# Performance work log

Measured on AMD Instinct MI355X. Metric: run time of the kernel, lower is better.

## Reference

```python
import jax, jax.numpy as jnp
import numpy as np

HEADS = 8
DIM_HEAD = 32
SCALE = DIM_HEAD ** -0.5
EPS = 1e-12  # F.normalize eps


def _rmsnorm_ch(t, g):
    # F.normalize(t, dim=1) * g * sqrt(C)  (normalize_dim=1)
    c = t.shape[1]
    norm = jnp.sqrt(jnp.sum(t * t, axis=1, keepdims=True))
    return t / jnp.maximum(norm, EPS) * g[None, :, None, None] * (c ** 0.5)


def setup_inputs() -> dict:
    key = jax.random.key(0)
    ks = jax.random.split(key, 4)
    B, C, H, W = 16, 256, 64, 64
    hidden = HEADS * DIM_HEAD  # 256
    x = jax.random.normal(ks[0], (B, C, H, W), dtype=jnp.float32)
    g1 = jnp.ones((C,), dtype=jnp.float32)
    # conv 1x1 weights stored as [out_ch, in_ch]
    w_qkv = jax.random.normal(ks[1], (hidden * 3, C), dtype=jnp.float32) * (1.0 / np.sqrt(C))
    w_out = jax.random.normal(ks[2], (C, hidden), dtype=jnp.float32) * (1.0 / np.sqrt(hidden))
    b_out = jnp.zeros((C,), dtype=jnp.float32)
    g2 = jnp.ones((C,), dtype=jnp.float32)
    return {"x": x, "g1": g1, "w_qkv": w_qkv, "w_out": w_out, "b_out": b_out, "g2": g2}


def reference(x, g1, w_qkv, w_out, b_out, g2):
    b, c, h, w = x.shape
    n = h * w
    xn = _rmsnorm_ch(x, g1)
    # 1x1 conv (no bias) == channel matmul
    qkv = jnp.einsum('oc,bchw->bohw', w_qkv, xn)
    q, k, v = jnp.split(qkv, 3, axis=1)
    # b (h c) x y -> b h c (x y)
    q = q.reshape(b, HEADS, DIM_HEAD, n)
    k = k.reshape(b, HEADS, DIM_HEAD, n)
    v = v.reshape(b, HEADS, DIM_HEAD, n)
    q = jax.nn.softmax(q, axis=-2) * SCALE  # softmax over dim_head
    k = jax.nn.softmax(k, axis=-1)          # softmax over sequence
    context = jnp.einsum('bhdn,bhen->bhde', k, v)  # [b,h,d,e] small
    out = jnp.einsum('bhde,bhdn->bhen', context, q)
    out = out.reshape(b, HEADS * DIM_HEAD, h, w)
    out = jnp.einsum('oc,bchw->bohw', w_out, out) + b_out[None, :, None, None]
    return _rmsnorm_ch(out, g2) + x
```

## Files before the change

### kernel.cpp

```cpp
#include <hip/hip_runtime.h>
#include <math.h>


#define B_ 16
#define C_ 256
#define N_ 4096
#define SCALE_ 0.17677669529663687f
#define EPS_ 1e-12f

typedef __attribute__((ext_vector_type(8))) short bf16x8;
typedef __attribute__((ext_vector_type(4))) float f32x4;

__device__ __forceinline__ ushort f2bf(float f) {
    union { float f; uint u; } x; x.f = f;
    uint r = (x.u + 0x7FFFu + ((x.u >> 16) & 1u)) >> 16;
    return (ushort)r;
}
__device__ __forceinline__ float bf2f(ushort s) {
    union { uint u; float f; } x; x.u = ((uint)s) << 16;
    return x.f;
}

__global__ __launch_bounds__(256) void k_prep(const float* __restrict__ w_qkv,
                                              const float* __restrict__ g1,
                                              ushort* __restrict__ Wp) {
    int o = blockIdx.x, c = threadIdx.x;
    Wp[(size_t)o * 256 + c] = f2bf(w_qkv[(size_t)o * 256 + c] * g1[c]);
}

__global__ __launch_bounds__(512) void k_kvctx(const ushort* __restrict__ Wp,
                                               const float* __restrict__ x,
                                               float* __restrict__ ctxp,
                                               float* __restrict__ sums_p) {
    extern __shared__ char lds[];
    ushort (*Asub)[40] = (ushort(*)[40])lds;
    char* BQ = lds + 20480;
    char* P  = lds + 86016;
    float* sspA  = (float*)(lds + 151552);
    float* rinvA = (float*)(lds + 153600);
    const int b = blockIdx.y, s = blockIdx.x;
    const int col0 = s * 128;
    const int t = threadIdx.x, l = t & 63, w = t >> 6;
    const int lr = l & 15, grp = l >> 4;
    const int wn = w & 3, wo = w >> 2;
    const float* xb = x + (size_t)b * C_ * N_ + col0;

    {
        int col = t & 127, rg = t >> 7;
        float ss = 0.f;
        #pragma unroll 8
        for (int i = 0; i < 64; ++i) {
            float v = xb[(size_t)(rg * 64 + i) * N_ + col];
            ss += v * v;
        }
        sspA[rg * 128 + col] = ss;
    }
    __syncthreads();
    if (t < 128)
        rinvA[t] = 16.f / fmaxf(sqrtf(sspA[t] + sspA[128 + t] + sspA[256 + t] + sspA[384 + t]), EPS_);
    __syncthreads();
    {
        int col = t & 127, rg = t >> 7;
        float rv = rinvA[col];
        uint sw = (uint)((col & 7) << 4);
        #pragma unroll
        for (int i = 0; i < 16; ++i) {
            int c = rg * 64 + i * 4;
            uint2 pk;
            pk.x = (uint)f2bf(xb[(size_t)c * N_ + col] * rv)
                 | ((uint)f2bf(xb[(size_t)(c + 1) * N_ + col] * rv) << 16);
            pk.y = (uint)f2bf(xb[(size_t)(c + 2) * N_ + col] * rv)
                 | ((uint)f2bf(xb[(size_t)(c + 3) * N_ + col] * rv) << 16);
            *(uint2*)(BQ + (((uint)(col * 512 + c * 2)) ^ sw)) = pk;
        }
    }

    #pragma unroll
    for (int p = 0; p < 2; ++p) {
        f32x4 acc[2][8] = {};
        for (int k0 = 0; k0 < 256; k0 += 32) {
            {
                int r = t >> 1, ko = (t & 1) * 16;
                const uint4* sa = (const uint4*)(Wp + (size_t)(256 + p * 256 + r) * 256 + k0 + ko);
                *(uint4*)&Asub[r][ko]     = sa[0];
                *(uint4*)&Asub[r][ko + 8] = sa[1];
            }
            __syncthreads();
            bf16x8 ax[2], bw[8];
            #pragma unroll
            for (int m = 0; m < 2; ++m) {
                int row = wn * 32 + m * 16 + lr;
                uint off = (uint)(row * 512 + (k0 + grp * 8) * 2) ^ (uint)((row & 7) << 4);
                ax[m] = *(const bf16x8*)(BQ + off);
            }
            #pragma unroll
            for (int nf = 0; nf < 8; ++nf)
                bw[nf] = *(const bf16x8*)&Asub[wo * 128 + nf * 16 + lr][grp * 8];
            #pragma unroll
            for (int m = 0; m < 2; ++m)
                #pragma unroll
                for (int nf = 0; nf < 8; ++nf)
                    acc[m][nf] = __builtin_amdgcn_mfma_f32_16x16x32_bf16(ax[m], bw[nf], acc[m][nf], 0, 0, 0);
            __syncthreads();
        }
        if (p == 0) {
            #pragma unroll
            for (int nf = 0; nf < 8; ++nf) {
                int d = wo * 128 + nf * 16 + lr;
                uint sw = (uint)((d & 7) << 4);
                #pragma unroll
                for (int m = 0; m < 2; ++m) {
                    int n0 = wn * 32 + m * 16 + grp * 4;
                    uint2 pk;
                    pk.x = (uint)f2bf(__expf(acc[m][nf][0])) | ((uint)f2bf(__expf(acc[m][nf][1])) << 16);
                    pk.y = (uint)f2bf(__expf(acc[m][nf][2])) | ((uint)f2bf(__expf(acc[m][nf][3])) << 16);
                    *(uint2*)(P + (((uint)(d * 256 + n0 * 2)) ^ sw)) = pk;
                }
            }
        } else {
            #pragma unroll
            for (int nf = 0; nf < 8; ++nf) {
                int e = wo * 128 + nf * 16 + lr;
                uint sw = (uint)((e & 7) << 4);
                #pragma unroll
                for (int m = 0; m < 2; ++m) {
                    int n0 = wn * 32 + m * 16 + grp * 4;
                    uint2 pk;
                    pk.x = (uint)f2bf(acc[m][nf][0]) | ((uint)f2bf(acc[m][nf][1]) << 16);
                    pk.y = (uint)f2bf(acc[m][nf][2]) | ((uint)f2bf(acc[m][nf][3]) << 16);
                    *(uint2*)(BQ + (((uint)(e * 256 + n0 * 2)) ^ sw)) = pk;
                }
            }
        }
    }
    __syncthreads();

    const int h = w;
    f32x4 c3[2][2] = {};
    f32x4 cS[2] = {};
    bf16x8 ones;
    #pragma unroll
    for (int j = 0; j < 8; ++j) ones[j] = (short)0x3F80;
    #pragma unroll
    for (int ks = 0; ks < 4; ++ks) {
        int n0 = ks * 32 + grp * 8;
        bf16x8 pA[2], vB[2];
        #pragma unroll
        for (int df = 0; df < 2; ++df) {
            int d = h * 32 + df * 16 + lr;
            pA[df] = *(const bf16x8*)(P + (((uint)(d * 256 + n0 * 2)) ^ ((uint)((d & 7) << 4))));
        }
        #pragma unroll
        for (int ef = 0; ef < 2; ++ef) {
            int e = h * 32 + ef * 16 + lr;
            vB[ef] = *(const bf16x8*)(BQ + (((uint)(e * 256 + n0 * 2)) ^ ((uint)((e & 7) << 4))));
        }
        #pragma unroll
        for (int df = 0; df < 2; ++df) {
            #pragma unroll
            for (int ef = 0; ef < 2; ++ef)
                c3[df][ef] = __builtin_amdgcn_mfma_f32_16x16x32_bf16(pA[df], vB[ef], c3[df][ef], 0, 0, 0);
            cS[df] = __builtin_amdgcn_mfma_f32_16x16x32_bf16(pA[df], ones, cS[df], 0, 0, 0);
        }
    }
    int bh = b * 8 + h;
    size_t base = ((size_t)s * 128 + bh) * 32;
    #pragma unroll
    for (int df = 0; df < 2; ++df) {
        #pragma unroll
        for (int ef = 0; ef < 2; ++ef)
            #pragma unroll
            for (int r = 0; r < 4; ++r)
                ctxp[(base + df * 16 + grp * 4 + r) * 32 + ef * 16 + lr] = c3[df][ef][r];
        if (lr == 0)
            #pragma unroll
            for (int r = 0; r < 4; ++r)
                sums_p[base + df * 16 + grp * 4 + r] = cS[df][r];
    }
}

__global__ __launch_bounds__(256) void k_fold(const float* __restrict__ w_out,
                                              const float* __restrict__ ctxp,
                                              const float* __restrict__ sums_p,
                                              ushort* __restrict__ M) {
    __shared__ float cn[32][33];
    __shared__ float sinv[32];
    int bh = blockIdx.x;
    int b = bh >> 3, h = bh & 7;
    int t = threadIdx.x;
    if (t < 32) {
        float st = 0.f;
        #pragma unroll 8
        for (int s = 0; s < 32; ++s) st += sums_p[(size_t)(s * 128 + bh) * 32 + t];
        sinv[t] = SCALE_ / st;
    }
    #pragma unroll
    for (int i = t; i < 1024; i += 256) {
        int d = i >> 5, e = i & 31;
        float cv = 0.f;
        #pragma unroll 8
        for (int s = 0; s < 32; ++s)
            cv += ctxp[((size_t)(s * 128 + bh) * 32 + d) * 32 + e];
        cn[e][d] = cv;
    }
    __syncthreads();
    float wreg[32];
    const float* wr = w_out + (size_t)t * 256 + h * 32;
    #pragma unroll
    for (int e = 0; e < 32; e += 4) {
        float4 wv = *(const float4*)&wr[e];
        wreg[e] = wv.x; wreg[e + 1] = wv.y; wreg[e + 2] = wv.z; wreg[e + 3] = wv.w;
    }
    float acc[32] = {};
    #pragma unroll
    for (int e = 0; e < 32; ++e) {
        float we = wreg[e];
        #pragma unroll
        for (int d = 0; d < 32; ++d) acc[d] += we * cn[e][d];
    }
    ushort* Mrow = M + ((size_t)b * 256 + t) * 256 + h * 32;
    #pragma unroll
    for (int d = 0; d < 32; ++d) Mrow[d] = f2bf(acc[d] * sinv[d]);
}

__global__ __launch_bounds__(512) void k_qfinal(const ushort* __restrict__ Wp,
                                                const ushort* __restrict__ M,
                                                const float* __restrict__ b_out,
                                                const float* __restrict__ g2,
                                                const float* __restrict__ x,
                                                float* __restrict__ out) {
    __shared__ __align__(16) char shmem[34816];
    __shared__ float ss2[8][64];
    __shared__ float rinvq[64];
    ushort* BQ = (ushort*)shmem;
    float*  OUT = (float*)shmem;
    const int b = blockIdx.y, col0 = blockIdx.x * 64;
    const int t = threadIdx.x, l = t & 63, w = t >> 6;
    const int lr = l & 15, grp = l >> 4;
    const float* xb2 = x + (size_t)b * C_ * N_;

    {
        int col = t & 63, rg = t >> 6;
        float ss = 0.f;
        #pragma unroll 8
        for (int i = 0; i < 32; ++i) {
            float v = xb2[(size_t)(rg * 32 + i) * N_ + col0 + col];
            ss += v * v;
        }
        ss2[rg][col] = ss;
    }
    __syncthreads();
    if (t < 64) {
        float st = ss2[0][t] + ss2[1][t] + ss2[2][t] + ss2[3][t]
                 + ss2[4][t] + ss2[5][t] + ss2[6][t] + ss2[7][t];
        rinvq[t] = 16.f / fmaxf(sqrtf(st), EPS_);
    }
    __syncthreads();
    {
        int col = t & 63, rg = t >> 6;
        float rv = rinvq[col];
        uint sw = (uint)((col & 7) << 4);
        #pragma unroll
        for (int i = 0; i < 8; ++i) {
            int c = rg * 32 + i * 4;
            uint2 pk;
            pk.x = (uint)f2bf(xb2[(size_t)c * N_ + col0 + col] * rv)
                 | ((uint)f2bf(xb2[(size_t)(c + 1) * N_ + col0 + col] * rv) << 16);
            pk.y = (uint)f2bf(xb2[(size_t)(c + 2) * N_ + col0 + col] * rv)
                 | ((uint)f2bf(xb2[(size_t)(c + 3) * N_ + col0 + col] * rv) << 16);
            *(uint2*)((char*)BQ + (((uint)(col * 512 + c * 2)) ^ sw)) = pk;
        }
    }
    __syncthreads();

    f32x4 acc[2][4] = {};
    for (int k0 = 0; k0 < 256; k0 += 32) {
        bf16x8 af[2], bf[4];
        #pragma unroll
        for (int m = 0; m < 2; ++m)
            af[m] = *(const bf16x8*)(Wp + (size_t)(w * 32 + m * 16 + lr) * 256 + k0 + grp * 8);
        #pragma unroll
        for (int n = 0; n < 4; ++n) {
            int row = n * 16 + lr;
            uint off = (uint)(row * 512 + (k0 + grp * 8) * 2) ^ (uint)((row & 7) << 4);
            bf[n] = *(const bf16x8*)((const char*)BQ + off);
        }
        #pragma unroll
        for (int m = 0; m < 2; ++m)
            #pragma unroll
            for (int n = 0; n < 4; ++n)
                acc[m][n] = __builtin_amdgcn_mfma_f32_16x16x32_bf16(af[m], bf[n], acc[m][n], 0, 0, 0);
    }
    __syncthreads();

    #pragma unroll
    for (int n = 0; n < 4; ++n) {
        float f[2][4];
        #pragma unroll
        for (int m = 0; m < 2; ++m)
            #pragma unroll
            for (int r = 0; r < 4; ++r) f[m][r] = acc[m][n][r];
        float mx = -1e30f;
        #pragma unroll
        for (int r = 0; r < 4; ++r) mx = fmaxf(mx, fmaxf(f[0][r], f[1][r]));
        mx = fmaxf(mx, __shfl_xor(mx, 16));
        mx = fmaxf(mx, __shfl_xor(mx, 32));
        float s = 0.f;
        #pragma unroll
        for (int r = 0; r < 4; ++r) {
            f[0][r] = __expf(f[0][r] - mx); s += f[0][r];
            f[1][r] = __expf(f[1][r] - mx); s += f[1][r];
        }
        s += __shfl_xor(s, 16); s += __shfl_xor(s, 32);
        float inv = 1.f / s;
        int cl = n * 16 + lr;
        #pragma unroll
        for (int m = 0; m < 2; ++m) {
            int d = w * 32 + m * 16 + grp * 4;
            uint2 pk;
            pk.x = (uint)f2bf(f[m][0] * inv) | ((uint)f2bf(f[m][1] * inv) << 16);
            pk.y = (uint)f2bf(f[m][2] * inv) | ((uint)f2bf(f[m][3] * inv) << 16);
            uint off = (uint)(cl * 512 + d * 2) ^ (uint)((cl & 7) << 4);
            *(uint2*)((char*)BQ + off) = pk;
        }
    }
    __syncthreads();

    f32x4 acc2[2][4] = {};
    const ushort* Mb = M + (size_t)b * 256 * 256;
    for (int k0 = 0; k0 < 256; k0 += 32) {
        bf16x8 af[2], bq[4];
        #pragma unroll
        for (int m = 0; m < 2; ++m)
            af[m] = *(const bf16x8*)(Mb + (size_t)(w * 32 + m * 16 + lr) * 256 + k0 + grp * 8);
        #pragma unroll
        for (int n = 0; n < 4; ++n) {
            int row = n * 16 + lr;
            uint off = (uint)(row * 512 + (k0 + grp * 8) * 2) ^ (uint)((row & 7) << 4);
            bq[n] = *(const bf16x8*)((const char*)BQ + off);
        }
        #pragma unroll
        for (int m = 0; m < 2; ++m)
            #pragma unroll
            for (int n = 0; n < 4; ++n)
                acc2[m][n] = __builtin_amdgcn_mfma_f32_16x16x32_bf16(af[m], bq[n], acc2[m][n], 0, 0, 0);
    }

    __syncthreads();
    #pragma unroll
    for (int n = 0; n < 4; ++n) {
        float local = 0.f;
        #pragma unroll
        for (int m = 0; m < 2; ++m) {
            int obase = w * 32 + m * 16 + grp * 4;
            #pragma unroll
            for (int r = 0; r < 4; ++r) {
                float f = acc2[m][n][r] + b_out[obase + r];
                acc2[m][n][r] = f;
                local += f * f;
            }
        }
        local += __shfl_xor(local, 16);
        local += __shfl_xor(local, 32);
        if (grp == 0) ss2[w][n * 16 + lr] = local;
    }
    __syncthreads();
    #pragma unroll
    for (int n = 0; n < 4; ++n) {
        int cl = n * 16 + lr;
        float tot = ss2[0][cl] + ss2[1][cl] + ss2[2][cl] + ss2[3][cl]
                  + ss2[4][cl] + ss2[5][cl] + ss2[6][cl] + ss2[7][cl];
        float rs = 16.f / fmaxf(sqrtf(tot), EPS_);
        #pragma unroll
        for (int m = 0; m < 2; ++m) {
            int obase = w * 32 + m * 16 + grp * 4;
            #pragma unroll
            for (int r = 0; r < 4; ++r)
                acc2[m][n][r] *= rs * g2[obase + r];
        }
    }
    float* ob = out + (size_t)b * C_ * N_;
    const int chunk = w >> 2;
    #pragma unroll
    for (int ch = 0; ch < 2; ++ch) {
        if (chunk == ch) {
            #pragma unroll
            for (int n = 0; n < 4; ++n) {
                int cl = n * 16 + lr;
                #pragma unroll
                for (int m = 0; m < 2; ++m) {
                    int rbase = (w & 3) * 32 + m * 16 + grp * 4;
                    #pragma unroll
                    for (int r = 0; r < 4; ++r)
                        OUT[(rbase + r) * 68 + cl] = acc2[m][n][r];
                }
            }
        }
        __syncthreads();
        #pragma unroll
        for (int i = 0; i < 4; ++i) {
            int rowl = i * 32 + (t >> 4);
            int grow = ch * 128 + rowl;
            float4 v = *(float4*)&OUT[rowl * 68 + (t & 15) * 4];
            float4 xr = *(const float4*)&xb2[(size_t)grow * N_ + col0 + (t & 15) * 4];
            v.x += xr.x; v.y += xr.y; v.z += xr.z; v.w += xr.w;
            *(float4*)&ob[(size_t)grow * N_ + col0 + (t & 15) * 4] = v;
        }
        __syncthreads();
    }
}

extern "C" void kernel_launch(void* const* d_in, const int* in_sizes, int n_in,
                              void* d_out, int out_size, void* d_ws, size_t ws_size,
                              hipStream_t stream) {
    const float* x     = (const float*)d_in[0];
    const float* g1    = (const float*)d_in[1];
    const float* w_qkv = (const float*)d_in[2];
    const float* w_out = (const float*)d_in[3];
    const float* b_out = (const float*)d_in[4];
    const float* g2    = (const float*)d_in[5];
    float* out = (float*)d_out;
    char* ws = (char*)d_ws;

    ushort* Wp     = (ushort*)(ws + 0);
    float*  ctxp   = (float*)(ws + 393216);
    float*  sums_p = (float*)(ws + 17170432);
    ushort* Mm     = (ushort*)(ws + 17694720);

    hipFuncSetAttribute((const void*)k_kvctx,
                        hipFuncAttributeMaxDynamicSharedMemorySize, 154112);

    k_prep<<<768, 256, 0, stream>>>(w_qkv, g1, Wp);
    k_kvctx<<<dim3(32, 16), 512, 154112, stream>>>(Wp, x, ctxp, sums_p);
    k_fold<<<128, 256, 0, stream>>>(w_out, ctxp, sums_p, Mm);
    k_qfinal<<<dim3(64, 16), 512, 0, stream>>>(Wp, Mm, b_out, g2, x, out);
}
```

Measured before the change: 133.8 us.

## Split kvctx column tile into two 64-column substeps and read weights from global

The k_kvctx kernel now processes its 128 columns in two sequential 64-column substeps and accumulates the context across them. It also drops the LDS staging buffer for the K/V weight rows, loading the MFMA B operands straight from global memory (L2 cached). Together these cut dynamic LDS from about 150KB to about 66KB, so more than one block can be resident per CU. The cost is uncoalesced, repeated global weight reads per wave, plus extra barriers and loop iterations.

```diff
diff --git a/kernel.cpp b/kernel.cpp
--- a/kernel.cpp
+++ b/kernel.cpp
@@ -33,137 +33,139 @@
                                                float* __restrict__ ctxp,
                                                float* __restrict__ sums_p) {
     extern __shared__ char lds[];
-    ushort (*Asub)[40] = (ushort(*)[40])lds;
-    char* BQ = lds + 20480;
-    char* P  = lds + 86016;
-    float* sspA  = (float*)(lds + 151552);
-    float* rinvA = (float*)(lds + 153600);
+    char* BQ = lds;
+    char* P  = lds + 32768;
+    float* sspA  = (float*)(lds + 65536);
+    float* rinvA = (float*)(lds + 67584);
     const int b = blockIdx.y, s = blockIdx.x;
-    const int col0 = s * 128;
     const int t = threadIdx.x, l = t & 63, w = t >> 6;
     const int lr = l & 15, grp = l >> 4;
-    const int wn = w & 3, wo = w >> 2;
-    const float* xb = x + (size_t)b * C_ * N_ + col0;
-
-    {
-        int col = t & 127, rg = t >> 7;
-        float ss = 0.f;
-        #pragma unroll 8
-        for (int i = 0; i < 64; ++i) {
-            float v = xb[(size_t)(rg * 64 + i) * N_ + col];
-            ss += v * v;
-        }
-        sspA[rg * 128 + col] = ss;
-    }
-    __syncthreads();
-    if (t < 128)
-        rinvA[t] = 16.f / fmaxf(sqrtf(sspA[t] + sspA[128 + t] + sspA[256 + t] + sspA[384 + t]), EPS_);
-    __syncthreads();
-    {
-        int col = t & 127, rg = t >> 7;
-        float rv = rinvA[col];
-        uint sw = (uint)((col & 7) << 4);
-        #pragma unroll
-        for (int i = 0; i < 16; ++i) {
-            int c = rg * 64 + i * 4;
-            uint2 pk;
-            pk.x = (uint)f2bf(xb[(size_t)c * N_ + col] * rv)
-                 | ((uint)f2bf(xb[(size_t)(c + 1) * N_ + col] * rv) << 16);
-            pk.y = (uint)f2bf(xb[(size_t)(c + 2) * N_ + col] * rv)
-                 | ((uint)f2bf(xb[(size_t)(c + 3) * N_ + col] * rv) << 16);
-            *(uint2*)(BQ + (((uint)(col * 512 + c * 2)) ^ sw)) = pk;
-        }
-    }
-
-    #pragma unroll
-    for (int p = 0; p < 2; ++p) {
-        f32x4 acc[2][8] = {};
-        for (int k0 = 0; k0 < 256; k0 += 32) {
-            {
-                int r = t >> 1, ko = (t & 1) * 16;
-                const uint4* sa = (const uint4*)(Wp + (size_t)(256 + p * 256 + r) * 256 + k0 + ko);
-                *(uint4*)&Asub[r][ko]     = sa[0];
-                *(uint4*)&Asub[r][ko + 8] = sa[1];
-            }
-            __syncthreads();
-            bf16x8 ax[2], bw[8];
-            #pragma unroll
-            for (int m = 0; m < 2; ++m) {
-                int row = wn * 32 + m * 16 + lr;
-                uint off = (uint)(row * 512 + (k0 + grp * 8) * 2) ^ (uint)((row & 7) << 4);
-                ax[m] = *(const bf16x8*)(BQ + off);
-            }
-            #pragma unroll
-            for (int nf = 0; nf < 8; ++nf)
-                bw[nf] = *(const bf16x8*)&Asub[wo * 128 + nf * 16 + lr][grp * 8];
-            #pragma unroll
-            for (int m = 0; m < 2; ++m)
-                #pragma unroll
-                for (int nf = 0; nf < 8; ++nf)
-                    acc[m][nf] = __builtin_amdgcn_mfma_f32_16x16x32_bf16(ax[m], bw[nf], acc[m][nf], 0, 0, 0);
-            __syncthreads();
-        }
-        if (p == 0) {
-            #pragma unroll
-            for (int nf = 0; nf < 8; ++nf) {
-                int d = wo * 128 + nf * 16 + lr;
-                uint sw = (uint)((d & 7) << 4);
-                #pragma unroll
-                for (int m = 0; m < 2; ++m) {
-                    int n0 = wn * 32 + m * 16 + grp * 4;
-                    uint2 pk;
-                    pk.x = (uint)f2bf(__expf(acc[m][nf][0])) | ((uint)f2bf(__expf(acc[m][nf][1])) << 16);
-                    pk.y = (uint)f2bf(__expf(acc[m][nf][2])) | ((uint)f2bf(__expf(acc[m][nf][3])) << 16);
-                    *(uint2*)(P + (((uint)(d * 256 + n0 * 2)) ^ sw)) = pk;
-                }
-            }
-        } else {
-            #pragma unroll
-            for (int nf = 0; nf < 8; ++nf) {
-                int e = wo * 128 + nf * 16 + lr;
-                uint sw = (uint)((e & 7) << 4);
-                #pragma unroll
-                for (int m = 0; m < 2; ++m) {
-                    int n0 = wn * 32 + m * 16 + grp * 4;
-                    uint2 pk;
-                    pk.x = (uint)f2bf(acc[m][nf][0]) | ((uint)f2bf(acc[m][nf][1]) << 16);
-                    pk.y = (uint)f2bf(acc[m][nf][2]) | ((uint)f2bf(acc[m][nf][3]) << 16);
-                    *(uint2*)(BQ + (((uint)(e * 256 + n0 * 2)) ^ sw)) = pk;
-                }
-            }
-        }
-    }
-    __syncthreads();
-
-    const int h = w;
+    const int wn = w & 1, wo = w >> 1;
+    const float* xb = x + (size_t)b * C_ * N_;
+
     f32x4 c3[2][2] = {};
     f32x4 cS[2] = {};
     bf16x8 ones;
     #pragma unroll
     for (int j = 0; j < 8; ++j) ones[j] = (short)0x3F80;
-    #pragma unroll
-    for (int ks = 0; ks < 4; ++ks) {
-        int n0 = ks * 32 + grp * 8;
-        bf16x8 pA[2], vB[2];
-        #pragma unroll
-        for (int df = 0; df < 2; ++df) {
-            int d = h * 32 + df * 16 + lr;
-            pA[df] = *(const bf16x8*)(P + (((uint)(d * 256 + n0 * 2)) ^ ((uint)((d & 7) << 4))));
-        }
-        #pragma unroll
-        for (int ef = 0; ef < 2; ++ef) {
-            int e = h * 32 + ef * 16 + lr;
-            vB[ef] = *(const bf16x8*)(BQ + (((uint)(e * 256 + n0 * 2)) ^ ((uint)((e & 7) << 4))));
-        }
-        #pragma unroll
-        for (int df = 0; df < 2; ++df) {
-            #pragma unroll
-            for (int ef = 0; ef < 2; ++ef)
-                c3[df][ef] = __builtin_amdgcn_mfma_f32_16x16x32_bf16(pA[df], vB[ef], c3[df][ef], 0, 0, 0);
-            cS[df] = __builtin_amdgcn_mfma_f32_16x16x32_bf16(pA[df], ones, cS[df], 0, 0, 0);
-        }
-    }
-    int bh = b * 8 + h;
+
+    #pragma unroll 1
+    for (int st = 0; st < 2; ++st) {
+        const int col0 = s * 128 + st * 64;
+        {
+            int col = t & 63, rg = t >> 6;
+            float ss = 0.f;
+            #pragma unroll 8
+            for (int i = 0; i < 32; ++i) {
+                float v = xb[(size_t)(rg * 32 + i) * N_ + col0 + col];
+                ss += v * v;
+            }
+            sspA[rg * 64 + col] = ss;
+        }
+        __syncthreads();
+        if (t < 64) {
+            float stot = sspA[t] + sspA[64 + t] + sspA[128 + t] + sspA[192 + t]
+                       + sspA[256 + t] + sspA[320 + t] + sspA[384 + t] + sspA[448 + t];
+            rinvA[t] = 16.f / fmaxf(sqrtf(stot), EPS_);
+        }
+        __syncthreads();
+        {
+            int col = t & 63, rg = t >> 6;
+            float rv = rinvA[col];
+            uint sw = (uint)((col & 7) << 4);
+            #pragma unroll
+            for (int i = 0; i < 8; ++i) {
+                int c = rg * 32 + i * 4;
+                uint2 pk;
+                pk.x = (uint)f2bf(xb[(size_t)c * N_ + col0 + col] * rv)
+                     | ((uint)f2bf(xb[(size_t)(c + 1) * N_ + col0 + col] * rv) << 16);
+                pk.y = (uint)f2bf(xb[(size_t)(c + 2) * N_ + col0 + col] * rv)
+                     | ((uint)f2bf(xb[(size_t)(c + 3) * N_ + col0 + col] * rv) << 16);
+                *(uint2*)(BQ + (((uint)(col * 512 + c * 2)) ^ sw)) = pk;
+            }
+        }
+        __syncthreads();
+
+        #pragma unroll
+        for (int p = 0; p < 2; ++p) {
+            f32x4 acc[2][4] = {};
+            for (int k0 = 0; k0 < 256; k0 += 32) {
+                bf16x8 ax[2], bw[4];
+                #pragma unroll
+                for (int m = 0; m < 2; ++m) {
+                    int row = wn * 32 + m * 16 + lr;
+                    uint off = (uint)(row * 512 + (k0 + grp * 8) * 2) ^ (uint)((row & 7) << 4);
+                    ax[m] = *(const bf16x8*)(BQ + off);
+                }
+                #pragma unroll
+                for (int nf = 0; nf < 4; ++nf)
+                    bw[nf] = *(const bf16x8*)(Wp + (size_t)(256 + p * 256 + wo * 64 + nf * 16 + lr) * 256 + k0 + grp * 8);
+                #pragma unroll
+                for (int m = 0; m < 2; ++m)
+                    #pragma unroll
+                    for (int nf = 0; nf < 4; ++nf)
+                        acc[m][nf] = __builtin_amdgcn_mfma_f32_16x16x32_bf16(ax[m], bw[nf], acc[m][nf], 0, 0, 0);
+            }
+            if (p == 0) {
+                #pragma unroll
+                for (int nf = 0; nf < 4; ++nf) {
+                    int d = wo * 64 + nf * 16 + lr;
+                    uint sw = (uint)((d & 7) << 4);
+                    #pragma unroll
+                    for (int m = 0; m < 2; ++m) {
+                        int n0 = wn * 32 + m * 16 + grp * 4;
+                        uint2 pk;
+                        pk.x = (uint)f2bf(__expf(acc[m][nf][0])) | ((uint)f2bf(__expf(acc[m][nf][1])) << 16);
+                        pk.y = (uint)f2bf(__expf(acc[m][nf][2])) | ((uint)f2bf(__expf(acc[m][nf][3])) << 16);
+                        *(uint2*)(P + (((uint)(d * 128 + n0 * 2)) ^ sw)) = pk;
+                    }
+                }
+            } else {
+                __syncthreads();
+                #pragma unroll
+                for (int nf = 0; nf < 4; ++nf) {
+                    int e = wo * 64 + nf * 16 + lr;
+                    uint sw = (uint)((e & 7) << 4);
+                    #pragma unroll
+                    for (int m = 0; m < 2; ++m) {
+                        int n0 = wn * 32 + m * 16 + grp * 4;
+                        uint2 pk;
+                        pk.x = (uint)f2bf(acc[m][nf][0]) | ((uint)f2bf(acc[m][nf][1]) << 16);
+                        pk.y = (uint)f2bf(acc[m][nf][2]) | ((uint)f2bf(acc[m][nf][3]) << 16);
+                        *(uint2*)(BQ + (((uint)(e * 128 + n0 * 2)) ^ sw)) = pk;
+                    }
+                }
+            }
+        }
+        __syncthreads();
+
+        const int h = w;
+        #pragma unroll
+        for (int ks = 0; ks < 2; ++ks) {
+            int n0 = ks * 32 + grp * 8;
+            bf16x8 pA[2], vB[2];
+            #pragma unroll
+            for (int df = 0; df < 2; ++df) {
+                int d = h * 32 + df * 16 + lr;
+                pA[df] = *(const bf16x8*)(P + (((uint)(d * 128 + n0 * 2)) ^ ((uint)((d & 7) << 4))));
+            }
+            #pragma unroll
+            for (int ef = 0; ef < 2; ++ef) {
+                int e = h * 32 + ef * 16 + lr;
+                vB[ef] = *(const bf16x8*)(BQ + (((uint)(e * 128 + n0 * 2)) ^ ((uint)((e & 7) << 4))));
+            }
+            #pragma unroll
+            for (int df = 0; df < 2; ++df) {
+                #pragma unroll
+                for (int ef = 0; ef < 2; ++ef)
+                    c3[df][ef] = __builtin_amdgcn_mfma_f32_16x16x32_bf16(pA[df], vB[ef], c3[df][ef], 0, 0, 0);
+                cS[df] = __builtin_amdgcn_mfma_f32_16x16x32_bf16(pA[df], ones, cS[df], 0, 0, 0);
+            }
+        }
+        __syncthreads();
+    }
+
+    int bh = b * 8 + w;
     size_t base = ((size_t)s * 128 + bh) * 32;
     #pragma unroll
     for (int df = 0; df < 2; ++df) {
@@ -428,10 +430,10 @@
     ushort* Mm     = (ushort*)(ws + 17694720);
 
     hipFuncSetAttribute((const void*)k_kvctx,
-                        hipFuncAttributeMaxDynamicSharedMemorySize, 154112);
+                        hipFuncAttributeMaxDynamicSharedMemorySize, 67840);
 
     k_prep<<<768, 256, 0, stream>>>(w_qkv, g1, Wp);
-    k_kvctx<<<dim3(32, 16), 512, 154112, stream>>>(Wp, x, ctxp, sums_p);
+    k_kvctx<<<dim3(32, 16), 512, 67840, stream>>>(Wp, x, ctxp, sums_p);
     k_fold<<<128, 256, 0, stream>>>(w_out, ctxp, sums_p, Mm);
     k_qfinal<<<dim3(64, 16), 512, 0, stream>>>(Wp, Mm, b_out, g2, x, out);
 }
```

Result: slower. 268.3 us (+100.4%).
